# Kernel tuning notes

Hardware: AMD Instinct MI355X
Metric: run time of the kernel (lower is better)

## Reference

```python
import jax, jax.numpy as jnp
import numpy as np

N_NODES = 50000


def gcn_conv(x, W, b, src, dst, norm, n):
    # PyG GCNConv: h = x W; out[dst] += norm * h[src]; out += b
    h = x @ W  # [N, out_dim]
    msg = h[src] * norm[:, None]  # [E+N, out_dim]
    out = jax.ops.segment_sum(msg, dst, num_segments=n)
    return out + b


def _norm_coeffs(src, dst, n):
    # symmetric normalization D^-1/2 A_hat D^-1/2 (self-loops already appended)
    deg = jax.ops.segment_sum(jnp.ones(src.shape[0], jnp.float32), dst, num_segments=n)
    dis = jnp.where(deg > 0, jax.lax.rsqrt(jnp.maximum(deg, 1.0)), 0.0)
    return dis[src] * dis[dst]


def setup_inputs() -> dict:
    key = jax.random.key(0)
    ks = jax.random.split(key, 8)
    n, e = N_NODES, 640000
    d_in, d_h, d_out = 128, 128, 64
    x = jax.random.normal(ks[0], (n, d_in), jnp.float32)
    edge_index = jax.random.randint(ks[1], (2, e), 0, n, jnp.int64)
    def glorot(k, shape):
        lim = np.sqrt(6.0 / (shape[0] + shape[1]))
        return jax.random.uniform(k, shape, jnp.float32, -lim, lim)
    return {
        "x": x,
        "edge_index": edge_index,
        "W1": glorot(ks[2], (d_in, d_h)), "b1": jnp.zeros((d_h,), jnp.float32),
        "W2": glorot(ks[3], (d_h, d_h)), "b2": jnp.zeros((d_h,), jnp.float32),
        "W3": glorot(ks[4], (d_h, d_out)), "b3": jnp.zeros((d_out,), jnp.float32),
    }


def reference(x, edge_index, W1, b1, W2, b2, W3, b3):
    n = x.shape[0]
    loop = jnp.arange(n, dtype=edge_index.dtype)
    src = jnp.concatenate([edge_index[0], loop])
    dst = jnp.concatenate([edge_index[1], loop])
    norm = _norm_coeffs(src, dst, n)
    h = jax.nn.relu(gcn_conv(x, W1, b1, src, dst, norm, n))
    h = jax.nn.relu(gcn_conv(h, W2, b2, src, dst, norm, n))
    return gcn_conv(h, W3, b3, src, dst, norm, n)
```

## Files before the change

### kernel.cpp

```cpp
#include <hip/hip_runtime.h>
#include <hip/hip_fp16.h>

typedef _Float16 f16x8 __attribute__((ext_vector_type(8)));
typedef float f32x4 __attribute__((ext_vector_type(4)));


__global__ void k_zero(int* __restrict__ p, int n) {
    int i = blockIdx.x * blockDim.x + threadIdx.x;
    if (i < n) p[i] = 0;
}

__global__ void k_ellfill(const int* __restrict__ src, const int* __restrict__ dst,
                          int* __restrict__ deg, int* __restrict__ ell, int E) {
    int e = blockIdx.x * blockDim.x + threadIdx.x;
    if (e >= E) return;
    int d = dst[e];
    int c = atomicAdd(&deg[d], 1);
    if (c < 64) ell[(size_t)d * 64 + c] = src[e];
}

template <int BN, int NT, bool IN_F32>
__global__ __launch_bounds__(256) void k_gemm_mfma(const void* __restrict__ Xv,
                                                   const float* __restrict__ W,
                                                   const int* __restrict__ deg,
                                                   _Float16* __restrict__ G, int N) {
    if (blockIdx.x == 0 && threadIdx.x < BN / 2) {
        ((int*)(G + (size_t)N * BN))[threadIdx.x] = 0;
    }

    const int lane = threadIdx.x & 63;
    const int wv = threadIdx.x >> 6;
    const int lo = lane & 15;
    const int kg = lane >> 4;
    const int colbase = wv * NT * 16;

    f16x8 b[4][NT];
#pragma unroll
    for (int t = 0; t < 4; ++t)
#pragma unroll
        for (int u = 0; u < NT; ++u)
#pragma unroll
            for (int j = 0; j < 8; ++j)
                b[t][u][j] = (_Float16)W[(size_t)(t * 32 + kg * 8 + j) * BN +
                                         colbase + u * 16 + lo];

    const float* Xf = (const float*)Xv;
    const _Float16* Xh = (const _Float16*)Xv;

    const int nslabs = N >> 4;
    for (int slab = blockIdx.x; slab < nslabs; slab += gridDim.x) {
        const int arow = slab * 16 + lo;
        f32x4 acc[NT];
#pragma unroll
        for (int u = 0; u < NT; ++u) acc[u] = (f32x4)0.0f;

#pragma unroll
        for (int t = 0; t < 4; ++t) {
            f16x8 a;
            if constexpr (IN_F32) {
                const float4* xp = (const float4*)&Xf[(size_t)arow * 128 + t * 32 + kg * 8];
                float4 u0 = xp[0], u1 = xp[1];
                a[0] = (_Float16)u0.x; a[1] = (_Float16)u0.y;
                a[2] = (_Float16)u0.z; a[3] = (_Float16)u0.w;
                a[4] = (_Float16)u1.x; a[5] = (_Float16)u1.y;
                a[6] = (_Float16)u1.z; a[7] = (_Float16)u1.w;
            } else {
                a = *(const f16x8*)&Xh[(size_t)arow * 128 + t * 32 + kg * 8];
            }
#pragma unroll
            for (int u = 0; u < NT; ++u)
                acc[u] = __builtin_amdgcn_mfma_f32_16x16x32_f16(a, b[t][u], acc[u], 0, 0, 0);
        }

        float ds[4];
#pragma unroll
        for (int r = 0; r < 4; ++r)
            ds[r] = rsqrtf((float)(deg[slab * 16 + kg * 4 + r] + 1));

#pragma unroll
        for (int u = 0; u < NT; ++u) {
            int col = colbase + u * 16 + lo;
#pragma unroll
            for (int r = 0; r < 4; ++r) {
                int row = slab * 16 + kg * 4 + r;
                G[(size_t)row * BN + col] = (_Float16)(acc[u][r] * ds[r]);
            }
        }
    }
}

__global__ __launch_bounds__(256) void k_aggr128(const int* __restrict__ deg,
                                                 const int* __restrict__ ell,
                                                 const __half* __restrict__ g,
                                                 const float* __restrict__ bias,
                                                 __half* __restrict__ out, int N) {
    int wid = blockIdx.x * 4 + (threadIdx.x >> 6);
    int lane = threadIdx.x & 63;
    if (wid >= N) return;
    int d = deg[wid];
    const int* row = &ell[(size_t)wid * 64];

    const __half2* gp = (const __half2*)g;
    float2 self = __half22float2(gp[(size_t)wid * 64 + lane]);
    float ax = self.x, ay = self.y;

    for (int j = 0; j < d; j += 16) {
        int idx[16];
        __half2 v[16];
#pragma unroll
        for (int t = 0; t < 16; ++t) {
            int jj = j + t;
            int c = row[min(jj, d - 1)];
            idx[t] = (jj < d) ? c : N;
        }
#pragma unroll
        for (int t = 0; t < 16; ++t) v[t] = gp[(size_t)idx[t] * 64 + lane];
#pragma unroll
        for (int t = 0; t < 16; ++t) {
            float2 f = __half22float2(v[t]);
            ax += f.x;
            ay += f.y;
        }
    }

    float di = rsqrtf((float)(d + 1));
    float2 bv = *(const float2*)&bias[lane * 2];
    ax = fmaxf(di * ax + bv.x, 0.f);
    ay = fmaxf(di * ay + bv.y, 0.f);
    ((__half2*)out)[(size_t)wid * 64 + lane] = __float22half2_rn(make_float2(ax, ay));
}

__global__ __launch_bounds__(256) void k_aggr64(const int* __restrict__ deg,
                                                const int* __restrict__ ell,
                                                const __half* __restrict__ g,
                                                const float* __restrict__ bias,
                                                float* __restrict__ out, int N) {
    int wid = blockIdx.x * 4 + (threadIdx.x >> 6);
    int lane = threadIdx.x & 63;
    if (wid >= N) return;
    int d = deg[wid];
    const int* row = &ell[(size_t)wid * 64];

    float a = __half2float(g[(size_t)wid * 64 + lane]);

    for (int j = 0; j < d; j += 16) {
        int idx[16];
        __half v[16];
#pragma unroll
        for (int t = 0; t < 16; ++t) {
            int jj = j + t;
            int c = row[min(jj, d - 1)];
            idx[t] = (jj < d) ? c : N;
        }
#pragma unroll
        for (int t = 0; t < 16; ++t) v[t] = g[(size_t)idx[t] * 64 + lane];
#pragma unroll
        for (int t = 0; t < 16; ++t) a += __half2float(v[t]);
    }

    out[(size_t)wid * 64 + lane] = rsqrtf((float)(d + 1)) * a + bias[lane];
}

extern "C" void kernel_launch(void* const* d_in, const int* in_sizes, int n_in,
                              void* d_out, int out_size, void* d_ws, size_t ws_size,
                              hipStream_t stream) {
    const float* x = (const float*)d_in[0];
    const int* ei = (const int*)d_in[1];
    const float* W1 = (const float*)d_in[2];
    const float* b1 = (const float*)d_in[3];
    const float* W2 = (const float*)d_in[4];
    const float* b2 = (const float*)d_in[5];
    const float* W3 = (const float*)d_in[6];
    const float* b3 = (const float*)d_in[7];

    const int N = in_sizes[0] / 128;
    const int E = in_sizes[1] / 2;
    const int* src = ei;
    const int* dst = ei + E;

    auto align512 = [](size_t x) { return (x + 511) & ~(size_t)511; };
    char* p = (char*)d_ws;
    int* deg = (int*)p;          p += align512((size_t)N * 4);
    int* ell = (int*)p;          p += align512((size_t)N * 64 * 4);
    __half* bufA = (__half*)p;   p += align512((size_t)(N + 1) * 128 * 2);
    __half* bufB = (__half*)p;

    k_zero<<<(N + 255) / 256, 256, 0, stream>>>(deg, N);
    k_ellfill<<<(E + 255) / 256, 256, 0, stream>>>(src, dst, deg, ell, E);

    const int ablocks = (N + 3) / 4;
    const int gemmBlocks = 512;

    k_gemm_mfma<128, 2, true><<<gemmBlocks, 256, 0, stream>>>(x, W1, deg, (_Float16*)bufA, N);
    k_aggr128<<<ablocks, 256, 0, stream>>>(deg, ell, bufA, b1, bufB, N);

    k_gemm_mfma<128, 2, false><<<gemmBlocks, 256, 0, stream>>>(bufB, W2, deg, (_Float16*)bufA, N);
    k_aggr128<<<ablocks, 256, 0, stream>>>(deg, ell, bufA, b2, bufB, N);

    k_gemm_mfma<64, 1, false><<<gemmBlocks, 256, 0, stream>>>(bufB, W3, deg, (_Float16*)bufA, N);
    k_aggr64<<<ablocks, 256, 0, stream>>>(deg, ell, bufA, b3, (float*)d_out, N);
}
```

Baseline: 165.2 us.

## Fuse ELL fill with first GEMM and aggregation with next-layer GEMM

Merges the edge-to-ELL fill into the first-layer GEMM kernel, and fuses each hidden-layer aggregation with the following layer's MFMA GEMM through a shared-memory tile. Because the first GEMM no longer knows degrees, the first aggregation applies the per-source normalisation inside the gather. ELL indices become 16-bit. This cuts the launch count and the round trip of the intermediate activations through global memory. In exchange it adds a degree lookup per neighbour in layer 1, assumes N fits in 16 bits and is a multiple of 16, and drops the grid-stride GEMM for one block per 16 rows.

```diff
diff --git a/kernel.cpp b/kernel.cpp
--- a/kernel.cpp
+++ b/kernel.cpp
@@ -10,23 +10,76 @@
     if (i < n) p[i] = 0;
 }
 
-__global__ void k_ellfill(const int* __restrict__ src, const int* __restrict__ dst,
-                          int* __restrict__ deg, int* __restrict__ ell, int E) {
-    int e = blockIdx.x * blockDim.x + threadIdx.x;
-    if (e >= E) return;
-    int d = dst[e];
-    int c = atomicAdd(&deg[d], 1);
-    if (c < 64) ell[(size_t)d * 64 + c] = src[e];
-}
-
-template <int BN, int NT, bool IN_F32>
-__global__ __launch_bounds__(256) void k_gemm_mfma(const void* __restrict__ Xv,
-                                                   const float* __restrict__ W,
-                                                   const int* __restrict__ deg,
-                                                   _Float16* __restrict__ G, int N) {
-    if (blockIdx.x == 0 && threadIdx.x < BN / 2) {
-        ((int*)(G + (size_t)N * BN))[threadIdx.x] = 0;
-    }
+__global__ __launch_bounds__(256) void k_fill_gemm1(
+    const float* __restrict__ X, const float* __restrict__ W,
+    const int* __restrict__ src, const int* __restrict__ dst,
+    int* __restrict__ deg, unsigned short* __restrict__ ell,
+    _Float16* __restrict__ H, int N, int E) {
+    if (blockIdx.x == 0 && threadIdx.x < 64)
+        ((int*)(H + (size_t)N * 128))[threadIdx.x] = 0;
+
+    const int lane = threadIdx.x & 63;
+    const int wv = threadIdx.x >> 6;
+    const int lo = lane & 15;
+    const int kg = lane >> 4;
+    const int colbase = wv * 32;
+
+    f16x8 b[4][2];
+#pragma unroll
+    for (int t = 0; t < 4; ++t)
+#pragma unroll
+        for (int u = 0; u < 2; ++u)
+#pragma unroll
+            for (int j = 0; j < 8; ++j)
+                b[t][u][j] = (_Float16)W[(size_t)(t * 32 + kg * 8 + j) * 128 +
+                                         colbase + u * 16 + lo];
+
+    const int nslabs = N >> 4;
+    for (int slab = blockIdx.x; slab < nslabs; slab += gridDim.x) {
+        const int arow = slab * 16 + lo;
+        f32x4 acc[2];
+        acc[0] = (f32x4)0.0f;
+        acc[1] = (f32x4)0.0f;
+#pragma unroll
+        for (int t = 0; t < 4; ++t) {
+            const float4* xp = (const float4*)&X[(size_t)arow * 128 + t * 32 + kg * 8];
+            float4 u0 = xp[0], u1 = xp[1];
+            f16x8 a;
+            a[0] = (_Float16)u0.x; a[1] = (_Float16)u0.y;
+            a[2] = (_Float16)u0.z; a[3] = (_Float16)u0.w;
+            a[4] = (_Float16)u1.x; a[5] = (_Float16)u1.y;
+            a[6] = (_Float16)u1.z; a[7] = (_Float16)u1.w;
+#pragma unroll
+            for (int u = 0; u < 2; ++u)
+                acc[u] = __builtin_amdgcn_mfma_f32_16x16x32_f16(a, b[t][u], acc[u], 0, 0, 0);
+        }
+#pragma unroll
+        for (int u = 0; u < 2; ++u) {
+            int col = colbase + u * 16 + lo;
+#pragma unroll
+            for (int r = 0; r < 4; ++r)
+                H[(size_t)(slab * 16 + kg * 4 + r) * 128 + col] = (_Float16)acc[u][r];
+        }
+    }
+
+    const int T = gridDim.x * blockDim.x;
+    for (int e = blockIdx.x * blockDim.x + threadIdx.x; e < E; e += T) {
+        int d = dst[e];
+        int c = atomicAdd(&deg[d], 1);
+        if (c < 64) ell[(size_t)d * 64 + c] = (unsigned short)src[e];
+    }
+}
+
+template <int BN, int NT, bool SCALE_SRC>
+__global__ __launch_bounds__(256) void k_aggr_gemm(
+    const __half* __restrict__ gin,
+    const int* __restrict__ deg, const unsigned short* __restrict__ ell,
+    const float* __restrict__ bias, const float* __restrict__ W,
+    _Float16* __restrict__ gout, int N) {
+    __shared__ _Float16 As[16][136];
+
+    if (blockIdx.x == 0 && threadIdx.x < BN / 2)
+        ((int*)(gout + (size_t)N * BN))[threadIdx.x] = 0;
 
     const int lane = threadIdx.x & 63;
     const int wv = threadIdx.x >> 6;
@@ -44,113 +97,104 @@
                 b[t][u][j] = (_Float16)W[(size_t)(t * 32 + kg * 8 + j) * BN +
                                          colbase + u * 16 + lo];
 
-    const float* Xf = (const float*)Xv;
-    const _Float16* Xh = (const _Float16*)Xv;
-
-    const int nslabs = N >> 4;
-    for (int slab = blockIdx.x; slab < nslabs; slab += gridDim.x) {
-        const int arow = slab * 16 + lo;
-        f32x4 acc[NT];
-#pragma unroll
-        for (int u = 0; u < NT; ++u) acc[u] = (f32x4)0.0f;
-
-#pragma unroll
-        for (int t = 0; t < 4; ++t) {
-            f16x8 a;
-            if constexpr (IN_F32) {
-                const float4* xp = (const float4*)&Xf[(size_t)arow * 128 + t * 32 + kg * 8];
-                float4 u0 = xp[0], u1 = xp[1];
-                a[0] = (_Float16)u0.x; a[1] = (_Float16)u0.y;
-                a[2] = (_Float16)u0.z; a[3] = (_Float16)u0.w;
-                a[4] = (_Float16)u1.x; a[5] = (_Float16)u1.y;
-                a[6] = (_Float16)u1.z; a[7] = (_Float16)u1.w;
-            } else {
-                a = *(const f16x8*)&Xh[(size_t)arow * 128 + t * 32 + kg * 8];
+    const __half2* gp = (const __half2*)gin;
+    const int base = blockIdx.x * 16;
+    for (int q = 0; q < 4; ++q) {
+        const int node = base + wv * 4 + q;
+        const int d = deg[node];
+        const int dc = min(d, 64);
+        const unsigned short* row = &ell[(size_t)node * 64];
+
+        float2 self = __half22float2(gp[(size_t)node * 64 + lane]);
+        float di = rsqrtf((float)(d + 1));
+        float ax, ay;
+        if constexpr (SCALE_SRC) {
+            ax = di * self.x;
+            ay = di * self.y;
+        } else {
+            ax = self.x;
+            ay = self.y;
+        }
+
+        for (int j = 0; j < dc; j += 16) {
+            int idx[16];
+            float w[16];
+            __half2 v[16];
+#pragma unroll
+            for (int t = 0; t < 16; ++t) {
+                int jj = j + t;
+                int c = row[min(jj, dc - 1)];
+                idx[t] = (jj < dc) ? c : N;
+                if constexpr (SCALE_SRC)
+                    w[t] = (jj < dc) ? rsqrtf((float)(deg[c] + 1)) : 0.0f;
             }
 #pragma unroll
-            for (int u = 0; u < NT; ++u)
-                acc[u] = __builtin_amdgcn_mfma_f32_16x16x32_f16(a, b[t][u], acc[u], 0, 0, 0);
-        }
-
-        float ds[4];
+            for (int t = 0; t < 16; ++t) v[t] = gp[(size_t)idx[t] * 64 + lane];
+#pragma unroll
+            for (int t = 0; t < 16; ++t) {
+                float2 f = __half22float2(v[t]);
+                if constexpr (SCALE_SRC) {
+                    ax += w[t] * f.x;
+                    ay += w[t] * f.y;
+                } else {
+                    ax += f.x;
+                    ay += f.y;
+                }
+            }
+        }
+
+        float2 bv = *(const float2*)&bias[lane * 2];
+        ax = fmaxf(di * ax + bv.x, 0.f);
+        ay = fmaxf(di * ay + bv.y, 0.f);
+        ((__half2*)&As[wv * 4 + q][0])[lane] = __float22half2_rn(make_float2(ax, ay));
+    }
+    __syncthreads();
+
+    f32x4 acc[NT];
+#pragma unroll
+    for (int u = 0; u < NT; ++u) acc[u] = (f32x4)0.0f;
+#pragma unroll
+    for (int t = 0; t < 4; ++t) {
+        f16x8 a = *(const f16x8*)&As[lo][t * 32 + kg * 8];
+#pragma unroll
+        for (int u = 0; u < NT; ++u)
+            acc[u] = __builtin_amdgcn_mfma_f32_16x16x32_f16(a, b[t][u], acc[u], 0, 0, 0);
+    }
+
+    float ds[4];
+#pragma unroll
+    for (int r = 0; r < 4; ++r) ds[r] = rsqrtf((float)(deg[base + kg * 4 + r] + 1));
+#pragma unroll
+    for (int u = 0; u < NT; ++u) {
+        int col = colbase + u * 16 + lo;
 #pragma unroll
         for (int r = 0; r < 4; ++r)
-            ds[r] = rsqrtf((float)(deg[slab * 16 + kg * 4 + r] + 1));
-
-#pragma unroll
-        for (int u = 0; u < NT; ++u) {
-            int col = colbase + u * 16 + lo;
-#pragma unroll
-            for (int r = 0; r < 4; ++r) {
-                int row = slab * 16 + kg * 4 + r;
-                G[(size_t)row * BN + col] = (_Float16)(acc[u][r] * ds[r]);
-            }
-        }
-    }
-}
-
-__global__ __launch_bounds__(256) void k_aggr128(const int* __restrict__ deg,
-                                                 const int* __restrict__ ell,
-                                                 const __half* __restrict__ g,
-                                                 const float* __restrict__ bias,
-                                                 __half* __restrict__ out, int N) {
+            gout[(size_t)(base + kg * 4 + r) * BN + col] = (_Float16)(acc[u][r] * ds[r]);
+    }
+}
+
+__global__ __launch_bounds__(256) void k_aggr_final(const int* __restrict__ deg,
+                                                    const unsigned short* __restrict__ ell,
+                                                    const __half* __restrict__ g,
+                                                    const float* __restrict__ bias,
+                                                    float* __restrict__ out, int N) {
     int wid = blockIdx.x * 4 + (threadIdx.x >> 6);
     int lane = threadIdx.x & 63;
     if (wid >= N) return;
     int d = deg[wid];
-    const int* row = &ell[(size_t)wid * 64];
-
-    const __half2* gp = (const __half2*)g;
-    float2 self = __half22float2(gp[(size_t)wid * 64 + lane]);
-    float ax = self.x, ay = self.y;
-
-    for (int j = 0; j < d; j += 16) {
+    int dc = min(d, 64);
+    const unsigned short* row = &ell[(size_t)wid * 64];
+
+    float a = __half2float(g[(size_t)wid * 64 + lane]);
+
+    for (int j = 0; j < dc; j += 16) {
         int idx[16];
-        __half2 v[16];
+        __half v[16];
 #pragma unroll
         for (int t = 0; t < 16; ++t) {
             int jj = j + t;
-            int c = row[min(jj, d - 1)];
-            idx[t] = (jj < d) ? c : N;
-        }
-#pragma unroll
-        for (int t = 0; t < 16; ++t) v[t] = gp[(size_t)idx[t] * 64 + lane];
-#pragma unroll
-        for (int t = 0; t < 16; ++t) {
-            float2 f = __half22float2(v[t]);
-            ax += f.x;
-            ay += f.y;
-        }
-    }
-
-    float di = rsqrtf((float)(d + 1));
-    float2 bv = *(const float2*)&bias[lane * 2];
-    ax = fmaxf(di * ax + bv.x, 0.f);
-    ay = fmaxf(di * ay + bv.y, 0.f);
-    ((__half2*)out)[(size_t)wid * 64 + lane] = __float22half2_rn(make_float2(ax, ay));
-}
-
-__global__ __launch_bounds__(256) void k_aggr64(const int* __restrict__ deg,
-                                                const int* __restrict__ ell,
-                                                const __half* __restrict__ g,
-                                                const float* __restrict__ bias,
-                                                float* __restrict__ out, int N) {
-    int wid = blockIdx.x * 4 + (threadIdx.x >> 6);
-    int lane = threadIdx.x & 63;
-    if (wid >= N) return;
-    int d = deg[wid];
-    const int* row = &ell[(size_t)wid * 64];
-
-    float a = __half2float(g[(size_t)wid * 64 + lane]);
-
-    for (int j = 0; j < d; j += 16) {
-        int idx[16];
-        __half v[16];
-#pragma unroll
-        for (int t = 0; t < 16; ++t) {
-            int jj = j + t;
-            int c = row[min(jj, d - 1)];
-            idx[t] = (jj < d) ? c : N;
+            int c = row[min(jj, dc - 1)];
+            idx[t] = (jj < dc) ? c : N;
         }
 #pragma unroll
         for (int t = 0; t < 16; ++t) v[t] = g[(size_t)idx[t] * 64 + lane];
@@ -178,25 +222,23 @@
     const int* src = ei;
     const int* dst = ei + E;
 
-    auto align512 = [](size_t x) { return (x + 511) & ~(size_t)511; };
+    auto align512 = [](size_t v) { return (v + 511) & ~(size_t)511; };
     char* p = (char*)d_ws;
-    int* deg = (int*)p;          p += align512((size_t)N * 4);
-    int* ell = (int*)p;          p += align512((size_t)N * 64 * 4);
-    __half* bufA = (__half*)p;   p += align512((size_t)(N + 1) * 128 * 2);
-    __half* bufB = (__half*)p;
+    int* deg = (int*)p;                        p += align512((size_t)N * 4);
+    unsigned short* ell = (unsigned short*)p;  p += align512((size_t)N * 64 * 2);
+    __half* h1 = (__half*)p;                   p += align512((size_t)(N + 1) * 128 * 2);
+    __half* g2 = (__half*)p;                   p += align512((size_t)(N + 1) * 128 * 2);
+    __half* g3 = (__half*)p;                   p += align512((size_t)(N + 1) * 64 * 2);
+
+    const int nslabBlocks = N / 16;
 
     k_zero<<<(N + 255) / 256, 256, 0, stream>>>(deg, N);
-    k_ellfill<<<(E + 255) / 256, 256, 0, stream>>>(src, dst, deg, ell, E);
-
-    const int ablocks = (N + 3) / 4;
-    const int gemmBlocks = 512;
-
-    k_gemm_mfma<128, 2, true><<<gemmBlocks, 256, 0, stream>>>(x, W1, deg, (_Float16*)bufA, N);
-    k_aggr128<<<ablocks, 256, 0, stream>>>(deg, ell, bufA, b1, bufB, N);
-
-    k_gemm_mfma<128, 2, false><<<gemmBlocks, 256, 0, stream>>>(bufB, W2, deg, (_Float16*)bufA, N);
-    k_aggr128<<<ablocks, 256, 0, stream>>>(deg, ell, bufA, b2, bufB, N);
-
-    k_gemm_mfma<64, 1, false><<<gemmBlocks, 256, 0, stream>>>(bufB, W3, deg, (_Float16*)bufA, N);
-    k_aggr64<<<ablocks, 256, 0, stream>>>(deg, ell, bufA, b3, (float*)d_out, N);
-}
+    k_fill_gemm1<<<1024, 256, 0, stream>>>(x, W1, src, dst, deg, ell,
+                                           (_Float16*)h1, N, E);
+    k_aggr_gemm<128, 2, true><<<nslabBlocks, 256, 0, stream>>>(
+        h1, deg, ell, b1, W2, (_Float16*)g2, N);
+    k_aggr_gemm<64, 1, false><<<nslabBlocks, 256, 0, stream>>>(
+        g2, deg, ell, b2, W3, (_Float16*)g3, N);
+    k_aggr_final<<<(N + 3) / 4, 256, 0, stream>>>(deg, ell, g3, b3,
+                                                  (float*)d_out, N);
+}
```

Measured after the change: 249.8 us. 51.3% more time.

## Pad degree counters, store ELL indices as uint16, halve final aggregation wavefront width

Applied to the files above, without the earlier changes.

Degree counters are padded to one per 64-byte stride so the atomics in the ELL fill do not contend on shared cache lines. ELL neighbour indices are stored as 16-bit values, which halves their footprint. The final 64-wide aggregation now uses 32 lanes per node with half2 loads, so each wavefront handles two nodes. Truncating indices to 16 bits is wrong for N=50000 sources above 65535? No: 50000 fits in uint16, but any larger graph would break, and the padding raises the memory used for degrees.

```diff
diff --git a/kernel.cpp b/kernel.cpp
--- a/kernel.cpp
+++ b/kernel.cpp
@@ -10,23 +10,24 @@
     if (i < n) p[i] = 0;
 }
 
-__global__ void k_ellfill(const int* __restrict__ src, const int* __restrict__ dst,
-                          int* __restrict__ deg, int* __restrict__ ell, int E) {
+__global__ __launch_bounds__(256) void k_ellfill(const int* __restrict__ src,
+                                                 const int* __restrict__ dst,
+                                                 int* __restrict__ deg32,
+                                                 unsigned short* __restrict__ ell, int E) {
     int e = blockIdx.x * blockDim.x + threadIdx.x;
     if (e >= E) return;
     int d = dst[e];
-    int c = atomicAdd(&deg[d], 1);
-    if (c < 64) ell[(size_t)d * 64 + c] = src[e];
+    int c = atomicAdd(&deg32[d << 4], 1);
+    if (c < 64) ell[(size_t)d * 64 + c] = (unsigned short)src[e];
 }
 
 template <int BN, int NT, bool IN_F32>
 __global__ __launch_bounds__(256) void k_gemm_mfma(const void* __restrict__ Xv,
                                                    const float* __restrict__ W,
-                                                   const int* __restrict__ deg,
+                                                   const int* __restrict__ deg32,
                                                    _Float16* __restrict__ G, int N) {
-    if (blockIdx.x == 0 && threadIdx.x < BN / 2) {
+    if (blockIdx.x == 0 && threadIdx.x < BN / 2)
         ((int*)(G + (size_t)N * BN))[threadIdx.x] = 0;
-    }
 
     const int lane = threadIdx.x & 63;
     const int wv = threadIdx.x >> 6;
@@ -75,7 +76,7 @@
         float ds[4];
 #pragma unroll
         for (int r = 0; r < 4; ++r)
-            ds[r] = rsqrtf((float)(deg[slab * 16 + kg * 4 + r] + 1));
+            ds[r] = rsqrtf((float)(deg32[(slab * 16 + kg * 4 + r) << 4] + 1));
 
 #pragma unroll
         for (int u = 0; u < NT; ++u) {
@@ -89,29 +90,30 @@
     }
 }
 
-__global__ __launch_bounds__(256) void k_aggr128(const int* __restrict__ deg,
-                                                 const int* __restrict__ ell,
-                                                 const __half* __restrict__ g,
+__global__ __launch_bounds__(256) void k_aggr128(const int* __restrict__ deg32,
+                                                 const unsigned short* __restrict__ ell,
+                                                 const __half* __restrict__ gin,
                                                  const float* __restrict__ bias,
                                                  __half* __restrict__ out, int N) {
     int wid = blockIdx.x * 4 + (threadIdx.x >> 6);
     int lane = threadIdx.x & 63;
     if (wid >= N) return;
-    int d = deg[wid];
-    const int* row = &ell[(size_t)wid * 64];
-
-    const __half2* gp = (const __half2*)g;
+    int d = deg32[wid << 4];
+    int dc = min(d, 64);
+    const unsigned short* row = &ell[(size_t)wid * 64];
+
+    const __half2* gp = (const __half2*)gin;
     float2 self = __half22float2(gp[(size_t)wid * 64 + lane]);
     float ax = self.x, ay = self.y;
 
-    for (int j = 0; j < d; j += 16) {
+    for (int j = 0; j < dc; j += 16) {
         int idx[16];
         __half2 v[16];
 #pragma unroll
         for (int t = 0; t < 16; ++t) {
             int jj = j + t;
-            int c = row[min(jj, d - 1)];
-            idx[t] = (jj < d) ? c : N;
+            int c = row[min(jj, dc - 1)];
+            idx[t] = (jj < dc) ? c : N;
         }
 #pragma unroll
         for (int t = 0; t < 16; ++t) v[t] = gp[(size_t)idx[t] * 64 + lane];
@@ -130,35 +132,47 @@
     ((__half2*)out)[(size_t)wid * 64 + lane] = __float22half2_rn(make_float2(ax, ay));
 }
 
-__global__ __launch_bounds__(256) void k_aggr64(const int* __restrict__ deg,
-                                                const int* __restrict__ ell,
-                                                const __half* __restrict__ g,
-                                                const float* __restrict__ bias,
-                                                float* __restrict__ out, int N) {
-    int wid = blockIdx.x * 4 + (threadIdx.x >> 6);
-    int lane = threadIdx.x & 63;
+__global__ __launch_bounds__(256) void k_aggr_final(const int* __restrict__ deg32,
+                                                    const unsigned short* __restrict__ ell,
+                                                    const __half* __restrict__ g,
+                                                    const float* __restrict__ bias,
+                                                    float* __restrict__ out, int N) {
+    int wid = blockIdx.x * 8 + (threadIdx.x >> 5);
+    int sub = threadIdx.x & 31;
     if (wid >= N) return;
-    int d = deg[wid];
-    const int* row = &ell[(size_t)wid * 64];
-
-    float a = __half2float(g[(size_t)wid * 64 + lane]);
-
-    for (int j = 0; j < d; j += 16) {
+    int d = deg32[wid << 4];
+    int dc = min(d, 64);
+    const unsigned short* row = &ell[(size_t)wid * 64];
+
+    const __half2* gp = (const __half2*)g;
+    float2 f0 = __half22float2(gp[(size_t)wid * 32 + sub]);
+    float ax = f0.x, ay = f0.y;
+
+    for (int j = 0; j < dc; j += 16) {
         int idx[16];
-        __half v[16];
+        __half2 v[16];
 #pragma unroll
         for (int t = 0; t < 16; ++t) {
             int jj = j + t;
-            int c = row[min(jj, d - 1)];
-            idx[t] = (jj < d) ? c : N;
-        }
-#pragma unroll
-        for (int t = 0; t < 16; ++t) v[t] = g[(size_t)idx[t] * 64 + lane];
-#pragma unroll
-        for (int t = 0; t < 16; ++t) a += __half2float(v[t]);
+            int c = row[min(jj, dc - 1)];
+            idx[t] = (jj < dc) ? c : N;
+        }
+#pragma unroll
+        for (int t = 0; t < 16; ++t) v[t] = gp[(size_t)idx[t] * 32 + sub];
+#pragma unroll
+        for (int t = 0; t < 16; ++t) {
+            float2 f = __half22float2(v[t]);
+            ax += f.x;
+            ay += f.y;
+        }
     }
 
-    out[(size_t)wid * 64 + lane] = rsqrtf((float)(d + 1)) * a + bias[lane];
+    float di = rsqrtf((float)(d + 1));
+    float2 bv = *(const float2*)&bias[sub * 2];
+    float2 o;
+    o.x = di * ax + bv.x;
+    o.y = di * ay + bv.y;
+    *(float2*)&out[(size_t)wid * 64 + sub * 2] = o;
 }
 
 extern "C" void kernel_launch(void* const* d_in, const int* in_sizes, int n_in,
@@ -178,25 +192,27 @@
     const int* src = ei;
     const int* dst = ei + E;
 
-    auto align512 = [](size_t x) { return (x + 511) & ~(size_t)511; };
+    auto align512 = [](size_t v) { return (v + 511) & ~(size_t)511; };
     char* p = (char*)d_ws;
-    int* deg = (int*)p;          p += align512((size_t)N * 4);
-    int* ell = (int*)p;          p += align512((size_t)N * 64 * 4);
-    __half* bufA = (__half*)p;   p += align512((size_t)(N + 1) * 128 * 2);
+    int* deg32 = (int*)p;                      p += align512((size_t)(N + 1) * 16 * 4);
+    unsigned short* ell = (unsigned short*)p;  p += align512((size_t)N * 64 * 2);
+    __half* bufA = (__half*)p;                 p += align512((size_t)(N + 1) * 128 * 2);
     __half* bufB = (__half*)p;
-
-    k_zero<<<(N + 255) / 256, 256, 0, stream>>>(deg, N);
-    k_ellfill<<<(E + 255) / 256, 256, 0, stream>>>(src, dst, deg, ell, E);
 
     const int ablocks = (N + 3) / 4;
     const int gemmBlocks = 512;
 
-    k_gemm_mfma<128, 2, true><<<gemmBlocks, 256, 0, stream>>>(x, W1, deg, (_Float16*)bufA, N);
-    k_aggr128<<<ablocks, 256, 0, stream>>>(deg, ell, bufA, b1, bufB, N);
-
-    k_gemm_mfma<128, 2, false><<<gemmBlocks, 256, 0, stream>>>(bufB, W2, deg, (_Float16*)bufA, N);
-    k_aggr128<<<ablocks, 256, 0, stream>>>(deg, ell, bufA, b2, bufB, N);
-
-    k_gemm_mfma<64, 1, false><<<gemmBlocks, 256, 0, stream>>>(bufB, W3, deg, (_Float16*)bufA, N);
-    k_aggr64<<<ablocks, 256, 0, stream>>>(deg, ell, bufA, b3, (float*)d_out, N);
-}
+    int zn = (N + 1) * 16;
+    k_zero<<<(zn + 255) / 256, 256, 0, stream>>>(deg32, zn);
+    k_ellfill<<<(E + 255) / 256, 256, 0, stream>>>(src, dst, deg32, ell, E);
+    k_gemm_mfma<128, 2, true><<<gemmBlocks, 256, 0, stream>>>(x, W1, deg32,
+                                                              (_Float16*)bufA, N);
+    k_aggr128<<<ablocks, 256, 0, stream>>>(deg32, ell, bufA, b1, bufB, N);
+    k_gemm_mfma<128, 2, false><<<gemmBlocks, 256, 0, stream>>>(bufB, W2, deg32,
+                                                               (_Float16*)bufA, N);
+    k_aggr128<<<ablocks, 256, 0, stream>>>(deg32, ell, bufA, b2, bufB, N);
+    k_gemm_mfma<64, 1, false><<<gemmBlocks, 256, 0, stream>>>(bufB, W3, deg32,
+                                                              (_Float16*)bufA, N);
+    k_aggr_final<<<(N + 7) / 8, 256, 0, stream>>>(deg32, ell, bufA, b3,
+                                                  (float*)d_out, N);
+}
```

Result: faster. 152.1 us (-7.9%).
